# Kernel tuning notes

Measured on AMD Instinct MI355X. Metric: run time of the kernel, lower is better.

The kernel has to match this reference:

```python
import jax, jax.numpy as jnp
import numpy as np
from jax import lax

B, T, N = 32, 48, 360   # batch, time steps, ROIs
H = 100                 # LSTM hidden (self.L)
D = 64                  # attention hidden (self.D)
K = 1                   # attention heads (self.K)
NUM_CLASS = 2


def setup_inputs() -> dict:
    key = jax.random.key(0)
    ks = jax.random.split(key, 14)
    s = 0.02
    return {
        "x": jax.random.normal(ks[0], (B, T, N, N), dtype=jnp.float32),
        # GCN: Linear(ROInum, 1) applied to (x @ I)
        "w_gcn": jax.random.normal(ks[1], (N,), dtype=jnp.float32) * s,
        "b_gcn": jnp.zeros((), dtype=jnp.float32),
        # LSTM (pytorch layout: [4H, in] with gate order i,f,g,o)
        "W_ih": jax.random.normal(ks[2], (4 * H, N), dtype=jnp.float32) * s,
        "W_hh": jax.random.normal(ks[3], (4 * H, H), dtype=jnp.float32) * s,
        "b_ih": jnp.zeros((4 * H,), dtype=jnp.float32),
        "b_hh": jnp.zeros((4 * H,), dtype=jnp.float32),
        # attention MLP: Linear(L,D) -> tanh -> Linear(D,K)
        "wa1": jax.random.normal(ks[4], (D, H), dtype=jnp.float32) * s,
        "ba1": jnp.zeros((D,), dtype=jnp.float32),
        "wa2": jax.random.normal(ks[5], (K, D), dtype=jnp.float32) * s,
        "ba2": jnp.zeros((K,), dtype=jnp.float32),
        # classifier: Linear(L*K, num_class) -> softmax (dropout inactive at eval)
        "wc": jax.random.normal(ks[6], (NUM_CLASS, H * K), dtype=jnp.float32) * s,
        "bc": jnp.zeros((NUM_CLASS,), dtype=jnp.float32),
    }


def _lstm(seq, W_ih, W_HH, b):
    # seq: [B, T, N] -> hidden states [B, T, H]
    def step(carry, xt):
        h, c = carry
        gates = xt @ W_ih.T + h @ W_HH.T + b  # [B, 4H]
        i, f, g, o = jnp.split(gates, 4, axis=-1)
        i, f, o = jax.nn.sigmoid(i), jax.nn.sigmoid(f), jax.nn.sigmoid(o)
        c = f * c + i * jnp.tanh(g)
        h = o * jnp.tanh(c)
        return (h, c), h

    h0 = jnp.zeros((seq.shape[0], H), seq.dtype)
    c0 = jnp.zeros((seq.shape[0], H), seq.dtype)
    _, hs = lax.scan(step, (h0, c0), jnp.swapaxes(seq, 0, 1))
    return jnp.swapaxes(hs, 0, 1)


def reference(x, w_gcn, b_gcn, W_ih, W_hh, b_ih, b_hh, wa1, ba1, wa2, ba2, wc, bc):
    # GCN per (sample, timestep): h = relu(Linear(x @ I)) == relu(x @ w + b)
    # batched over B and T in one einsum (eliminates the python loops).
    gout = jax.nn.relu(jnp.einsum("btnm,m->btn", x, w_gcn) + b_gcn)  # [B,T,N]

    out = _lstm(gout, W_ih, W_hh, b_ih + b_hh)  # [B,T,H]

    # MIL attention: A = Linear(tanh(Linear(out)))
    A = jnp.tanh(jnp.einsum("bth,dh->btd", out, wa1) + ba1)
    A = jnp.einsum("btd,kd->btk", A, wa2) + ba2          # [B,T,K]
    A = jnp.swapaxes(A, 2, 1)                             # [B,K,T]
    Att = A
    A = jax.nn.softmax(A, axis=2)
    M = jnp.einsum("bkt,bth->bkh", A, out).reshape(x.shape[0], H * K)

    Y_prob = jax.nn.softmax(M @ wc.T + bc, axis=1)  # dropout is identity at eval
    return (Y_prob, Att)
```

## Files before the change

### kernel.cpp

```cpp
#include <hip/hip_runtime.h>
#include <math.h>

#define BB 32
#define TT 48
#define NN 360
#define HH 100
#define DD 64
#define NC 2
#define G4 400

typedef float vf4 __attribute__((ext_vector_type(4)));

__device__ __forceinline__ float sigmoid_fast(float x) {
    return 1.f / (1.f + __expf(-x));
}
__device__ __forceinline__ float tanh_fast(float x) {
    float ax = fabsf(x);
    float e = __expf(-2.f * ax);
    float t = (1.f - e) / (1.f + e);
    return copysignf(t, x);
}
__device__ __forceinline__ float dot4v(vf4 a, float4 b) {
    return a.x*b.x + a.y*b.y + a.z*b.z + a.w*b.w;
}
__device__ __forceinline__ float bcast_lane(float v, int l) {
    return __int_as_float(__builtin_amdgcn_readlane(__float_as_int(v), l));
}
__device__ __forceinline__ vf4 ntload4(const float* p) {
    return __builtin_nontemporal_load((const vf4*)p);
}

#define DPP_ADD(x, ctrl, rmask) \
    x += __int_as_float(__builtin_amdgcn_update_dpp(0, __float_as_int(x), ctrl, rmask, 0xf, true));
#define WAVE_RED(p) \
    DPP_ADD(p, 0x111, 0xf) DPP_ADD(p, 0x112, 0xf) DPP_ADD(p, 0x114, 0xf) DPP_ADD(p, 0x118, 0xf) \
    DPP_ADD(p, 0x142, 0xa) DPP_ADD(p, 0x143, 0xc)

__global__ __launch_bounds__(256) void gcn_kernel(const float* __restrict__ x,
                                                  const float* __restrict__ w,
                                                  const float* __restrict__ bptr,
                                                  float* __restrict__ gout, int nquads) {
    int tid = threadIdx.x;
    int lane = tid & 63;
    int wv = tid >> 6;
    float4 wa = ((const float4*)w)[lane];
    float4 wb = (lane < 26) ? ((const float4*)w)[lane + 64] : make_float4(0.f, 0.f, 0.f, 0.f);
    float b = bptr[0];
    int stride = 4 * gridDim.x;
    for (int q = blockIdx.x * 4 + wv; q < nquads; q += stride) {
        int row0 = 4 * q;
        const float* x0 = x + (size_t)(row0 + 0) * NN;
        const float* x1 = x + (size_t)(row0 + 1) * NN;
        const float* x2 = x + (size_t)(row0 + 2) * NN;
        const float* x3 = x + (size_t)(row0 + 3) * NN;
        vf4 a0 = ntload4(x0 + 4*lane);
        vf4 a1 = ntload4(x1 + 4*lane);
        vf4 a2 = ntload4(x2 + 4*lane);
        vf4 a3 = ntload4(x3 + 4*lane);
        float p0 = dot4v(a0, wa);
        float p1 = dot4v(a1, wa);
        float p2 = dot4v(a2, wa);
        float p3 = dot4v(a3, wa);
        if (lane < 26) {
            vf4 b0 = ntload4(x0 + 4*(lane + 64));
            vf4 b1 = ntload4(x1 + 4*(lane + 64));
            vf4 b2 = ntload4(x2 + 4*(lane + 64));
            vf4 b3 = ntload4(x3 + 4*(lane + 64));
            p0 += dot4v(b0, wb);
            p1 += dot4v(b1, wb);
            p2 += dot4v(b2, wb);
            p3 += dot4v(b3, wb);
        }
        WAVE_RED(p0)
        WAVE_RED(p1)
        WAVE_RED(p2)
        WAVE_RED(p3)
        if (lane == 63) {
            float4 r;
            r.x = fmaxf(p0 + b, 0.f);
            r.y = fmaxf(p1 + b, 0.f);
            r.z = fmaxf(p2 + b, 0.f);
            r.w = fmaxf(p3 + b, 0.f);
            ((float4*)gout)[q] = r;
        }
    }
}

__global__ void transpose_wih(const float* __restrict__ Wih, float* __restrict__ Wt2) {
    int idx = blockIdx.x * blockDim.x + threadIdx.x;
    if (idx < NN * G4) {
        int j = idx / NN, n = idx % NN;
        Wt2[n * G4 + 2 * (j % 200) + (j / 200)] = Wih[idx];
    }
}

__global__ __launch_bounds__(256) void xproj_kernel(const float* __restrict__ gout,
                                                    const float* __restrict__ Wt2,
                                                    const float* __restrict__ b_ih,
                                                    const float* __restrict__ b_hh,
                                                    float* __restrict__ xproj) {
    int tid = threadIdx.x;
    if (tid >= 200) return;
    int r0 = blockIdx.x * 4;
    float acc00 = 0.f, acc01 = 0.f, acc10 = 0.f, acc11 = 0.f;
    float acc20 = 0.f, acc21 = 0.f, acc30 = 0.f, acc31 = 0.f;
    const float* g0p = gout + (size_t)(r0 + 0) * NN;
    const float* g1p = gout + (size_t)(r0 + 1) * NN;
    const float* g2p = gout + (size_t)(r0 + 2) * NN;
    const float* g3p = gout + (size_t)(r0 + 3) * NN;
    const float* wp = Wt2 + 2 * tid;
    for (int n = 0; n < NN; n += 4) {
        float4 g0 = *(const float4*)(g0p + n);
        float4 g1 = *(const float4*)(g1p + n);
        float4 g2 = *(const float4*)(g2p + n);
        float4 g3 = *(const float4*)(g3p + n);
        float2 wA = *(const float2*)(wp + (n + 0) * G4);
        float2 wB = *(const float2*)(wp + (n + 1) * G4);
        float2 wC = *(const float2*)(wp + (n + 2) * G4);
        float2 wD = *(const float2*)(wp + (n + 3) * G4);
        acc00 += g0.x*wA.x + g0.y*wB.x + g0.z*wC.x + g0.w*wD.x;
        acc01 += g0.x*wA.y + g0.y*wB.y + g0.z*wC.y + g0.w*wD.y;
        acc10 += g1.x*wA.x + g1.y*wB.x + g1.z*wC.x + g1.w*wD.x;
        acc11 += g1.x*wA.y + g1.y*wB.y + g1.z*wC.y + g1.w*wD.y;
        acc20 += g2.x*wA.x + g2.y*wB.x + g2.z*wC.x + g2.w*wD.x;
        acc21 += g2.x*wA.y + g2.y*wB.y + g2.z*wC.y + g2.w*wD.y;
        acc30 += g3.x*wA.x + g3.y*wB.x + g3.z*wC.x + g3.w*wD.x;
        acc31 += g3.x*wA.y + g3.y*wB.y + g3.z*wC.y + g3.w*wD.y;
    }
    float bias0 = b_ih[tid] + b_hh[tid];
    float bias1 = b_ih[tid + 200] + b_hh[tid + 200];
    xproj[(size_t)(r0 + 0) * G4 + tid]       = acc00 + bias0;
    xproj[(size_t)(r0 + 0) * G4 + tid + 200] = acc01 + bias1;
    xproj[(size_t)(r0 + 1) * G4 + tid]       = acc10 + bias0;
    xproj[(size_t)(r0 + 1) * G4 + tid + 200] = acc11 + bias1;
    xproj[(size_t)(r0 + 2) * G4 + tid]       = acc20 + bias0;
    xproj[(size_t)(r0 + 2) * G4 + tid + 200] = acc21 + bias1;
    xproj[(size_t)(r0 + 3) * G4 + tid]       = acc30 + bias0;
    xproj[(size_t)(r0 + 3) * G4 + tid + 200] = acc31 + bias1;
}

__global__ __launch_bounds__(448) void lstm_attn_kernel(const float* __restrict__ xproj,
                                                        const float* __restrict__ Whh,
                                                        const float* __restrict__ wa1,
                                                        const float* __restrict__ ba1,
                                                        const float* __restrict__ wa2,
                                                        const float* __restrict__ ba2,
                                                        const float* __restrict__ wc,
                                                        const float* __restrict__ bc,
                                                        float* __restrict__ out) {
    __shared__ __align__(16) float ho[TT * HH];
    __shared__ __align__(16) float h_lds[128];
    __shared__ float gates[G4];
    __shared__ float sc[TT];
    __shared__ float p[TT];
    __shared__ float M[HH];
    int b = blockIdx.x;
    int tid = threadIdx.x;
    int lane = tid & 63;
    float wr[HH];
    if (tid < G4) {
        #pragma unroll
        for (int k = 0; k < HH; k++) wr[k] = Whh[tid * HH + k];
    }
    float c = 0.f;
    if (tid < 128) h_lds[tid] = 0.f;
    float xp = (tid < G4) ? xproj[(size_t)(b * TT) * G4 + tid] : 0.f;
    __syncthreads();
    for (int t = 0; t < TT; t++) {
        float xp_next = (tid < G4 && t + 1 < TT)
                      ? xproj[(size_t)(b * TT + t + 1) * G4 + tid] : 0.f;
        float ha = h_lds[lane];
        float hb = h_lds[64 + lane];
        if (tid < G4) {
            float s0 = 0.f, s1 = 0.f, s2 = 0.f, s3 = 0.f;
            #pragma unroll
            for (int k = 0; k < 64; k += 4) {
                s0 += bcast_lane(ha, k+0) * wr[k+0];
                s1 += bcast_lane(ha, k+1) * wr[k+1];
                s2 += bcast_lane(ha, k+2) * wr[k+2];
                s3 += bcast_lane(ha, k+3) * wr[k+3];
            }
            #pragma unroll
            for (int k = 64; k < 100; k += 4) {
                s0 += bcast_lane(hb, k-64) * wr[k+0];
                s1 += bcast_lane(hb, k-63) * wr[k+1];
                s2 += bcast_lane(hb, k-62) * wr[k+2];
                s3 += bcast_lane(hb, k-61) * wr[k+3];
            }
            gates[tid] = xp + (s0 + s1) + (s2 + s3);
        }
        __syncthreads();
        if (tid < HH) {
            float ig = sigmoid_fast(gates[tid]);
            float fg = sigmoid_fast(gates[tid + HH]);
            float gg = tanh_fast(gates[tid + 2*HH]);
            float og = sigmoid_fast(gates[tid + 3*HH]);
            c = fg * c + ig * gg;
            float hh = og * tanh_fast(c);
            h_lds[tid] = hh;
            ho[t * HH + tid] = hh;
        }
        xp = xp_next;
        __syncthreads();
    }
    int wave = tid >> 6;
    for (int t = wave; t < TT; t += 7) {
        float a = 0.f;
        if (lane < DD) {
            float s = ba1[lane];
            #pragma unroll
            for (int h2 = 0; h2 < HH; h2 += 4) {
                float4 h4v = *(const float4*)&ho[t*HH + h2];
                s += wa1[lane*HH + h2+0]*h4v.x + wa1[lane*HH + h2+1]*h4v.y
                   + wa1[lane*HH + h2+2]*h4v.z + wa1[lane*HH + h2+3]*h4v.w;
            }
            a = tanh_fast(s) * wa2[lane];
        }
        #pragma unroll
        for (int off = 32; off; off >>= 1) a += __shfl_down(a, off, 64);
        if (lane == 0) sc[t] = a + ba2[0];
    }
    __syncthreads();
    if (tid < 64) {
        float v = (lane < TT) ? sc[lane] : -1e30f;
        if (lane < TT) out[BB*NC + b*TT + lane] = v;
        float m = v;
        #pragma unroll
        for (int off = 32; off; off >>= 1) m = fmaxf(m, __shfl_xor(m, off, 64));
        float e = (lane < TT) ? __expf(v - m) : 0.f;
        float s = e;
        #pragma unroll
        for (int off = 32; off; off >>= 1) s += __shfl_xor(s, off, 64);
        if (lane < TT) p[lane] = e / s;
    }
    __syncthreads();
    if (tid < HH) {
        float m = 0.f;
        #pragma unroll
        for (int t = 0; t < TT; t++) m += p[t] * ho[t*HH + tid];
        M[tid] = m;
    }
    __syncthreads();
    if (tid == 0) {
        float l0 = bc[0], l1 = bc[1];
        for (int h2 = 0; h2 < HH; h2++) { l0 += M[h2]*wc[h2]; l1 += M[h2]*wc[HH + h2]; }
        float mx = fmaxf(l0, l1);
        float e0 = __expf(l0 - mx), e1 = __expf(l1 - mx);
        float s = e0 + e1;
        out[b*NC + 0] = e0 / s;
        out[b*NC + 1] = e1 / s;
    }
}

extern "C" void kernel_launch(void* const* d_in, const int* in_sizes, int n_in,
                              void* d_out, int out_size, void* d_ws, size_t ws_size,
                              hipStream_t stream) {
    const float* x     = (const float*)d_in[0];
    const float* w_gcn = (const float*)d_in[1];
    const float* b_gcn = (const float*)d_in[2];
    const float* W_ih  = (const float*)d_in[3];
    const float* W_hh  = (const float*)d_in[4];
    const float* b_ih  = (const float*)d_in[5];
    const float* b_hh  = (const float*)d_in[6];
    const float* wa1   = (const float*)d_in[7];
    const float* ba1   = (const float*)d_in[8];
    const float* wa2   = (const float*)d_in[9];
    const float* ba2   = (const float*)d_in[10];
    const float* wc    = (const float*)d_in[11];
    const float* bc    = (const float*)d_in[12];
    float* out = (float*)d_out;
    float* ws  = (float*)d_ws;

    float* gout  = ws;
    float* Wt2   = gout + 552960;
    float* xproj = Wt2 + 144000;

    int nquads = BB * TT * NN / 4;
    transpose_wih<<<(NN*G4 + 255)/256, 256, 0, stream>>>(W_ih, Wt2);
    gcn_kernel<<<2048, 256, 0, stream>>>(x, w_gcn, b_gcn, gout, nquads);
    xproj_kernel<<<384, 256, 0, stream>>>(gout, Wt2, b_ih, b_hh, xproj);
    lstm_attn_kernel<<<BB, 448, 0, stream>>>(xproj, W_hh, wa1, ba1, wa2, ba2, wc, bc, out);
}
```

Measured before the change: 222.1 us.

## Software-pipeline GCN row loads with double-buffered registers and LDS restaging

The GCN reduction kernel now has each wave handle groups of 8 contiguous rows (a 2880-float chunk). It loads each chunk with fully coalesced 256-float strides into two register sets, so the next two groups' loads are in flight while the current group is computed. Data is restaged through per-wave LDS so each row's dot product can be read back at row offsets. The grid is reduced to 768 blocks. This aims to raise memory-level parallelism on the dominant x read (~212 MB), at the cost of heavy register use, LDS traffic and possible occupancy loss.

```diff
diff --git a/kernel.cpp b/kernel.cpp
--- a/kernel.cpp
+++ b/kernel.cpp
@@ -20,14 +20,14 @@
     float t = (1.f - e) / (1.f + e);
     return copysignf(t, x);
 }
-__device__ __forceinline__ float dot4v(vf4 a, float4 b) {
-    return a.x*b.x + a.y*b.y + a.z*b.z + a.w*b.w;
-}
 __device__ __forceinline__ float bcast_lane(float v, int l) {
     return __int_as_float(__builtin_amdgcn_readlane(__float_as_int(v), l));
 }
 __device__ __forceinline__ vf4 ntload4(const float* p) {
     return __builtin_nontemporal_load((const vf4*)p);
+}
+__device__ __forceinline__ float dotslot(vf4 a, vf4 w) {
+    return fmaf(a.w, w.w, fmaf(a.z, w.z, fmaf(a.y, w.y, a.x * w.x)));
 }
 
 #define DPP_ADD(x, ctrl, rmask) \
@@ -36,53 +36,91 @@
     DPP_ADD(p, 0x111, 0xf) DPP_ADD(p, 0x112, 0xf) DPP_ADD(p, 0x114, 0xf) DPP_ADD(p, 0x118, 0xf) \
     DPP_ADD(p, 0x142, 0xa) DPP_ADD(p, 0x143, 0xc)
 
+#define RG 8
+#define NGROUPS (BB*TT*NN/RG)
+#define GF4 (RG*NN/4)
+#define LOADG(S, gidx) do { if ((gidx) < NGROUPS) { \
+    const float* gb_ = x + (size_t)(gidx) * (RG * NN); \
+    S##0  = ntload4(gb_ + 0*256  + 4*lane); \
+    S##1  = ntload4(gb_ + 1*256  + 4*lane); \
+    S##2  = ntload4(gb_ + 2*256  + 4*lane); \
+    S##3  = ntload4(gb_ + 3*256  + 4*lane); \
+    S##4  = ntload4(gb_ + 4*256  + 4*lane); \
+    S##5  = ntload4(gb_ + 5*256  + 4*lane); \
+    S##6  = ntload4(gb_ + 6*256  + 4*lane); \
+    S##7  = ntload4(gb_ + 7*256  + 4*lane); \
+    S##8  = ntload4(gb_ + 8*256  + 4*lane); \
+    S##9  = ntload4(gb_ + 9*256  + 4*lane); \
+    S##10 = ntload4(gb_ + 10*256 + 4*lane); \
+    if (lane < 16) S##11 = ntload4(gb_ + 11*256 + 4*lane); \
+} } while (0)
+#define WRITELDS(S) do { \
+    buf[0*64  + lane] = S##0; \
+    buf[1*64  + lane] = S##1; \
+    buf[2*64  + lane] = S##2; \
+    buf[3*64  + lane] = S##3; \
+    buf[4*64  + lane] = S##4; \
+    buf[5*64  + lane] = S##5; \
+    buf[6*64  + lane] = S##6; \
+    buf[7*64  + lane] = S##7; \
+    buf[8*64  + lane] = S##8; \
+    buf[9*64  + lane] = S##9; \
+    buf[10*64 + lane] = S##10; \
+    if (lane < 16) buf[11*64 + lane] = S##11; \
+} while (0)
+#define COMPUTE_STORE(gcur) do { \
+    float s_[RG]; \
+    _Pragma("unroll") \
+    for (int r = 0; r < RG; ++r) { \
+        vf4 a_ = buf[r*90 + lane]; \
+        float p_ = dotslot(a_, wa); \
+        if (lane < 26) { vf4 a2_ = buf[r*90 + 64 + lane]; p_ += dotslot(a2_, wb); } \
+        WAVE_RED(p_) \
+        s_[r] = p_; \
+    } \
+    if (lane == 63) { \
+        float4 o0_, o1_; \
+        o0_.x = fmaxf(s_[0] + b, 0.f); o0_.y = fmaxf(s_[1] + b, 0.f); \
+        o0_.z = fmaxf(s_[2] + b, 0.f); o0_.w = fmaxf(s_[3] + b, 0.f); \
+        o1_.x = fmaxf(s_[4] + b, 0.f); o1_.y = fmaxf(s_[5] + b, 0.f); \
+        o1_.z = fmaxf(s_[6] + b, 0.f); o1_.w = fmaxf(s_[7] + b, 0.f); \
+        ((float4*)gout)[2*(gcur)]     = o0_; \
+        ((float4*)gout)[2*(gcur) + 1] = o1_; \
+    } \
+} while (0)
+
 __global__ __launch_bounds__(256) void gcn_kernel(const float* __restrict__ x,
                                                   const float* __restrict__ w,
                                                   const float* __restrict__ bptr,
-                                                  float* __restrict__ gout, int nquads) {
+                                                  float* __restrict__ gout) {
+    __shared__ __align__(16) vf4 sbuf[4][GF4];
     int tid = threadIdx.x;
     int lane = tid & 63;
     int wv = tid >> 6;
-    float4 wa = ((const float4*)w)[lane];
-    float4 wb = (lane < 26) ? ((const float4*)w)[lane + 64] : make_float4(0.f, 0.f, 0.f, 0.f);
+    vf4* buf = sbuf[wv];
+    vf4 wa = *(const vf4*)(w + 4*lane);
+    vf4 wb;
+    if (lane < 26) wb = *(const vf4*)(w + 4*(64 + lane));
+    else { wb.x = 0.f; wb.y = 0.f; wb.z = 0.f; wb.w = 0.f; }
     float b = bptr[0];
-    int stride = 4 * gridDim.x;
-    for (int q = blockIdx.x * 4 + wv; q < nquads; q += stride) {
-        int row0 = 4 * q;
-        const float* x0 = x + (size_t)(row0 + 0) * NN;
-        const float* x1 = x + (size_t)(row0 + 1) * NN;
-        const float* x2 = x + (size_t)(row0 + 2) * NN;
-        const float* x3 = x + (size_t)(row0 + 3) * NN;
-        vf4 a0 = ntload4(x0 + 4*lane);
-        vf4 a1 = ntload4(x1 + 4*lane);
-        vf4 a2 = ntload4(x2 + 4*lane);
-        vf4 a3 = ntload4(x3 + 4*lane);
-        float p0 = dot4v(a0, wa);
-        float p1 = dot4v(a1, wa);
-        float p2 = dot4v(a2, wa);
-        float p3 = dot4v(a3, wa);
-        if (lane < 26) {
-            vf4 b0 = ntload4(x0 + 4*(lane + 64));
-            vf4 b1 = ntload4(x1 + 4*(lane + 64));
-            vf4 b2 = ntload4(x2 + 4*(lane + 64));
-            vf4 b3 = ntload4(x3 + 4*(lane + 64));
-            p0 += dot4v(b0, wb);
-            p1 += dot4v(b1, wb);
-            p2 += dot4v(b2, wb);
-            p3 += dot4v(b3, wb);
-        }
-        WAVE_RED(p0)
-        WAVE_RED(p1)
-        WAVE_RED(p2)
-        WAVE_RED(p3)
-        if (lane == 63) {
-            float4 r;
-            r.x = fmaxf(p0 + b, 0.f);
-            r.y = fmaxf(p1 + b, 0.f);
-            r.z = fmaxf(p2 + b, 0.f);
-            r.w = fmaxf(p3 + b, 0.f);
-            ((float4*)gout)[q] = r;
-        }
+    const int gstride = gridDim.x * 4;
+    int g = blockIdx.x * 4 + wv;
+    vf4 sa0, sa1, sa2, sa3, sa4, sa5, sa6, sa7, sa8, sa9, sa10, sa11;
+    vf4 sb0, sb1, sb2, sb3, sb4, sb5, sb6, sb7, sb8, sb9, sb10, sb11;
+    LOADG(sa, g);
+    LOADG(sb, g + gstride);
+    for (int g2 = g; g2 < NGROUPS; ) {
+        __builtin_amdgcn_sched_barrier(0);
+        WRITELDS(sa);
+        LOADG(sa, g2 + 2*gstride);
+        COMPUTE_STORE(g2);
+        g2 += gstride;
+        if (g2 >= NGROUPS) break;
+        __builtin_amdgcn_sched_barrier(0);
+        WRITELDS(sb);
+        LOADG(sb, g2 + 2*gstride);
+        COMPUTE_STORE(g2);
+        g2 += gstride;
     }
 }
 
@@ -275,9 +313,8 @@
     float* Wt2   = gout + 552960;
     float* xproj = Wt2 + 144000;
 
-    int nquads = BB * TT * NN / 4;
     transpose_wih<<<(NN*G4 + 255)/256, 256, 0, stream>>>(W_ih, Wt2);
-    gcn_kernel<<<2048, 256, 0, stream>>>(x, w_gcn, b_gcn, gout, nquads);
+    gcn_kernel<<<768, 256, 0, stream>>>(x, w_gcn, b_gcn, gout);
     xproj_kernel<<<384, 256, 0, stream>>>(gout, Wt2, b_ih, b_hh, xproj);
     lstm_attn_kernel<<<BB, 448, 0, stream>>>(xproj, W_hh, wa1, ba1, wa2, ba2, wc, bc, out);
 }
```

Measured after the change: 213.8 us. -3.7%, faster.
